# Performance work log

Measured on AMD Instinct MI355X. Metric: run time of the kernel, lower is better.

The kernel has to match this reference:

```python
import jax, jax.numpy as jnp
import numpy as np
import math

D = 256; H = 8; L = 6; DK = D // H

def _ln(x, g, b):
    m = jnp.mean(x, -1, keepdims=True)
    v = jnp.mean((x - m) ** 2, -1, keepdims=True)
    return (x - m) * jax.lax.rsqrt(v + 1e-5) * g + b

def setup_inputs() -> dict:
    key = jax.random.key(0)
    ks = jax.random.split(key, 16)
    B, N, F, E = 8, 768, 128, 4
    s = 0.02
    inp = {}
    inp['node_feats'] = jax.random.normal(ks[0], (B, N, F), jnp.float32)
    inp['adj'] = jax.random.randint(ks[1], (B, N, N), 0, 2, jnp.int32)
    inp['dist'] = jax.random.uniform(ks[2], (B, N, N), jnp.float32)
    inp['edge_type_oh'] = jax.random.uniform(ks[3], (B, N, N, E), jnp.float32)
    inp['node_proj_w'] = jax.random.normal(ks[4], (F, D), jnp.float32) * s
    inp['node_proj_b'] = jnp.zeros((D,), jnp.float32)
    inp['cls'] = jax.random.normal(ks[5], (1, 1, D), jnp.float32) * s
    inp['etw'] = jax.random.normal(ks[6], (E,), jnp.float32) * s
    inp['noedge_bias'] = jnp.float32(-2.0)
    inp['deg_scale'] = jnp.float32(0.2)
    inp['gamma'] = jnp.float32(0.8)
    inp['v2n'] = jnp.float32(0.1)
    inp['n2v'] = jnp.float32(0.1)
    inp['vself'] = jnp.float32(0.05)
    inp['ln1_g'] = jnp.ones((L, D), jnp.float32); inp['ln1_b'] = jnp.zeros((L, D), jnp.float32)
    inp['qw'] = jax.random.normal(ks[7], (L, D, D), jnp.float32) * s; inp['qb'] = jnp.zeros((L, D), jnp.float32)
    inp['kw'] = jax.random.normal(ks[8], (L, D, D), jnp.float32) * s; inp['kb'] = jnp.zeros((L, D), jnp.float32)
    inp['vw'] = jax.random.normal(ks[9], (L, D, D), jnp.float32) * s; inp['vb'] = jnp.zeros((L, D), jnp.float32)
    inp['ow'] = jax.random.normal(ks[10], (L, D, D), jnp.float32) * s; inp['ob'] = jnp.zeros((L, D), jnp.float32)
    inp['ln2_g'] = jnp.ones((L, D), jnp.float32); inp['ln2_b'] = jnp.zeros((L, D), jnp.float32)
    Dm = int(D * 1.0)  # mlp_ratio=1.0
    inp['fc1w'] = jax.random.normal(ks[11], (L, D, Dm), jnp.float32) * s; inp['fc1b'] = jnp.zeros((L, Dm), jnp.float32)
    inp['fc2w'] = jax.random.normal(ks[12], (L, Dm, D), jnp.float32) * s; inp['fc2b'] = jnp.zeros((L, D), jnp.float32)
    return inp

def _build_bias(adj_f, dist, edge_type_oh, etw, noedge_bias, deg_scale, gamma, v2n, n2v, vself):
    # DynamicAttnBiasBuilder: hard_mask=False, use_degree=True, vnode_spd_mode='replace', gamma != 0
    B, N, _ = adj_f.shape
    T = N + 1
    e = jnp.einsum('bije,e->bij', edge_type_oh, etw) - gamma * dist  # (B,N,N)
    e = jnp.where(adj_f > 0, e, e + noedge_bias)
    deg = adj_f.sum(-1)  # (B,N)
    deg_norm = (deg[:, :, None] + deg[:, None, :]) / (deg.max(axis=1, keepdims=True)[:, :, None] + 1e-6)
    e = e + deg_scale * deg_norm
    bias = jnp.zeros((B, T, T), jnp.float32)
    bias = bias.at[:, 1:, 1:].set(e)
    bias = bias.at[:, 0, 1:].set(v2n)   # vnode_spd_mode == 'replace'
    bias = bias.at[:, 1:, 0].set(n2v)
    bias = bias.at[:, 0, 0].set(vself)
    return bias  # (B,T,T), broadcast over heads

def _mhsa(x, bias, qw, qb, kw, kb, vw, vb, ow, ob):
    B, T, _ = x.shape
    q = (x @ qw + qb).reshape(B, T, H, DK).transpose(0, 2, 1, 3)
    k = (x @ kw + kb).reshape(B, T, H, DK).transpose(0, 2, 1, 3)
    v = (x @ vw + vb).reshape(B, T, H, DK).transpose(0, 2, 1, 3)
    scores = jnp.einsum('bhqd,bhkd->bhqk', q, k) / math.sqrt(DK)
    scores = scores + bias[:, None, :, :]
    attn = jax.nn.softmax(scores, axis=-1)
    out = jnp.einsum('bhqk,bhkd->bhqd', attn, v)
    out = out.transpose(0, 2, 1, 3).reshape(B, T, D)
    return out @ ow + ob

def _forward(node_feats, adj, dist, edge_type_oh, node_proj_w, node_proj_b, cls,
             etw, noedge_bias, deg_scale, gamma, v2n, n2v, vself,
             ln1_g, ln1_b, qw, qb, kw, kb, vw, vb, ow, ob,
             ln2_g, ln2_b, fc1w, fc1b, fc2w, fc2b):
    adj_f = adj.astype(jnp.float32)
    bias = _build_bias(adj_f, dist, edge_type_oh, etw, noedge_bias, deg_scale, gamma, v2n, n2v, vself)
    B = node_feats.shape[0]
    x = node_feats @ node_proj_w + node_proj_b  # (B,N,D)
    x = jnp.concatenate([jnp.broadcast_to(cls, (B, 1, D)), x], axis=1)  # prepend virtual node -> (B,T,D)
    for l in range(L):
        h = _mhsa(_ln(x, ln1_g[l], ln1_b[l]), bias, qw[l], qb[l], kw[l], kb[l], vw[l], vb[l], ow[l], ob[l])
        x = x + h
        m = _ln(x, ln2_g[l], ln2_b[l])
        m = jax.nn.gelu(m @ fc1w[l] + fc1b[l], approximate=False) @ fc2w[l] + fc2b[l]
        x = x + m
    return x

def reference(node_feats, adj, dist, edge_type_oh, node_proj_w, node_proj_b, cls,
              etw, noedge_bias, deg_scale, gamma, v2n, n2v, vself,
              ln1_g, ln1_b, qw, qb, kw, kb, vw, vb, ow, ob,
              ln2_g, ln2_b, fc1w, fc1b, fc2w, fc2b):
    return _forward(node_feats, adj, dist, edge_type_oh, node_proj_w, node_proj_b, cls,
                    etw, noedge_bias, deg_scale, gamma, v2n, n2v, vself,
                    ln1_g, ln1_b, qw, qb, kw, kb, vw, vb, ow, ob,
                    ln2_g, ln2_b, fc1w, fc1b, fc2w, fc2b)
```

## Files before the change

kernel.cpp:

```cpp
#include <hip/hip_runtime.h>
#include <math.h>

#define BB 8
#define NN 768
#define TT 769
#define DD 256
#define HH 8
#define DKK 32
#define FF 128
#define LL 6
#define MM 6152
#define SCALE 0.17677669529663687f
#define TP 832
#define GBP 776
#define BSP 792
#define HP 264
#define WSZ 65536

typedef __attribute__((ext_vector_type(8))) short s16x8;
typedef __attribute__((ext_vector_type(8))) unsigned short u16x8;
typedef __attribute__((ext_vector_type(4))) float f32x4;

__device__ inline short f2bf(float x) {
    unsigned u = __float_as_uint(x);
    unsigned r = (u + 0x7FFFu + ((u >> 16) & 1u)) >> 16;
    return (short)r;
}
__device__ inline float bf2f(unsigned short s) {
    return __uint_as_float(((unsigned)s) << 16);
}
__device__ inline float gelu_f(float x) {
    return 0.5f * x * (1.f + erff(x * 0.70710678118654752f));
}

__global__ __launch_bounds__(256) void deg_kernel(const int* __restrict__ adj,
                                                  float* __restrict__ deg) {
    int row  = blockIdx.x * 4 + (threadIdx.x >> 6);
    int lane = threadIdx.x & 63;
    const int* p = adj + (size_t)row * NN;
    int s = 0;
#pragma unroll
    for (int i = 0; i < NN / 64; ++i) s += p[lane + 64 * i];
#pragma unroll
    for (int off = 32; off > 0; off >>= 1) s += __shfl_xor(s, off);
    if (lane == 0) deg[row] = (float)s;
}

__global__ __launch_bounds__(256) void degmax_kernel(const float* __restrict__ deg,
                                                     float* __restrict__ dmax) {
    __shared__ float red[256];
    int b = blockIdx.x, t = threadIdx.x;
    float m = 0.f;
    for (int i = t; i < NN; i += 256) m = fmaxf(m, deg[b * NN + i]);
    red[t] = m;
    __syncthreads();
    for (int s = 128; s > 0; s >>= 1) {
        if (t < s) red[t] = fmaxf(red[t], red[t + s]);
        __syncthreads();
    }
    if (t == 0) dmax[b] = red[0];
}

__global__ __launch_bounds__(256) void bias_kernel(
    const float* __restrict__ dist, const float* __restrict__ eoh,
    const int* __restrict__ adj, const float* __restrict__ deg,
    const float* __restrict__ dmax, const float* __restrict__ etw,
    const float* __restrict__ noedge, const float* __restrict__ degsc,
    const float* __restrict__ gamma, const float* __restrict__ v2n,
    const float* __restrict__ n2v, const float* __restrict__ vself,
    unsigned short* __restrict__ bias)
{
    long long idx = (long long)blockIdx.x * 256 + threadIdx.x;
    const long long total = (long long)BB * TT * GBP;
    if (idx >= total) return;
    int b  = (int)(idx / ((long long)TT * GBP));
    int r  = (int)(idx % ((long long)TT * GBP));
    int qi = r / GBP, kj = r % GBP;
    float out;
    if (kj >= TT)                out = 0.f;
    else if (qi == 0 && kj == 0) out = vself[0];
    else if (qi == 0)            out = v2n[0];
    else if (kj == 0)            out = n2v[0];
    else {
        int i = qi - 1, j = kj - 1;
        size_t e = ((size_t)b * NN + i) * NN + j;
        float4 oh = *(const float4*)(eoh + 4 * e);
        float val = oh.x * etw[0] + oh.y * etw[1] + oh.z * etw[2] + oh.w * etw[3]
                    - gamma[0] * dist[e];
        if (adj[e] == 0) val += noedge[0];
        val += degsc[0] * (deg[b * NN + i] + deg[b * NN + j]) / (dmax[b] + 1e-6f);
        out = val;
    }
    bias[idx] = (unsigned short)f2bf(out);
}

__global__ __launch_bounds__(256) void nodeproj_ln_kernel(
    const float* __restrict__ nf, const float* __restrict__ w,
    const float* __restrict__ bsv, const float* __restrict__ cls,
    const float* __restrict__ g, const float* __restrict__ bvec,
    float* __restrict__ x, short* __restrict__ xn)
{
    __shared__ float sf[FF];
    __shared__ float red[256];
    int row = blockIdx.x, t = threadIdx.x;
    int b = row / TT, tr = row % TT;
    float y;
    if (tr == 0) {
        y = cls[t];
    } else {
        if (t < FF) sf[t] = nf[((size_t)b * NN + tr - 1) * FF + t];
        __syncthreads();
        y = bsv[t];
#pragma unroll 8
        for (int kk = 0; kk < FF; ++kk) y = fmaf(sf[kk], w[kk * DD + t], y);
    }
    x[(size_t)row * DD + t] = y;
    red[t] = y;
    __syncthreads();
    for (int s = 128; s > 0; s >>= 1) { if (t < s) red[t] += red[t + s]; __syncthreads(); }
    float mean = red[0] * (1.f / DD);
    __syncthreads();
    float d = y - mean;
    red[t] = d * d;
    __syncthreads();
    for (int s = 128; s > 0; s >>= 1) { if (t < s) red[t] += red[t + s]; __syncthreads(); }
    float var = red[0] * (1.f / DD);
    xn[(size_t)row * DD + t] = f2bf(d * rsqrtf(var + 1e-5f) * g[t] + bvec[t]);
}

__global__ __launch_bounds__(256) void wtrans_kernel(
    const float* __restrict__ qw, const float* __restrict__ kw,
    const float* __restrict__ vw, const float* __restrict__ ow,
    const float* __restrict__ f1w, const float* __restrict__ f2w,
    short* __restrict__ wt2)
{
    int mi = blockIdx.x >> 4, kg = blockIdx.x & 15;
    int fam = mi / 6, l = mi % 6;
    const float* W;
    if      (fam == 0) W = qw;
    else if (fam == 1) W = kw;
    else if (fam == 2) W = vw;
    else if (fam == 3) W = ow;
    else if (fam == 4) W = f1w;
    else               W = f2w;
    W += (size_t)l * DD * DD;
    int n = threadIdx.x;
    short* out = wt2 + (size_t)mi * WSZ;
#pragma unroll
    for (int kk = 0; kk < 16; ++kk) {
        int k = kg * 16 + kk;
        float val = W[(size_t)k * DD + n];
        size_t idx = (size_t)(((n >> 4) * 8 + (k >> 5)) * 512
                   + (((k >> 3) & 3) * 16 + (n & 15)) * 8 + (k & 7));
        out[idx] = f2bf(val);
    }
}

__global__ __launch_bounds__(256) void gemm_qkv_kernel(
    const short* __restrict__ A, const short* __restrict__ wtl,
    const float* __restrict__ qb, const float* __restrict__ kb,
    const float* __restrict__ vb,
    short* __restrict__ qo, short* __restrict__ ko, short* __restrict__ vtb)
{
    int t = threadIdx.x;
    int w = t >> 6, lane = t & 63, quad = lane >> 4, m16 = lane & 15;
    int m0 = blockIdx.x * 16;
    int fam = blockIdx.y;
    const short* Wf = wtl + (size_t)fam * 6 * WSZ;
    const float* bsv = fam == 0 ? qb : (fam == 1 ? kb : vb);
    int arow = m0 + m16; if (arow >= MM) arow = MM - 1;
    const short* ap = A + (size_t)arow * DD + quad * 8;
    const short* wbase = Wf + (size_t)(w * 4) * 4096 + lane * 8;
    f32x4 acc[4] = {};
#pragma unroll
    for (int kc = 0; kc < 8; ++kc) {
        s16x8 af = *(const s16x8*)(ap + kc * 32);
#pragma unroll
        for (int nt = 0; nt < 4; ++nt) {
            s16x8 bf = *(const s16x8*)(wbase + (size_t)nt * 4096 + kc * 512);
            acc[nt] = __builtin_amdgcn_mfma_f32_16x16x32_bf16(af, bf, acc[nt], 0, 0, 0);
        }
    }
    if (fam < 2) {
        short* outp = fam == 0 ? qo : ko;
#pragma unroll
        for (int nt = 0; nt < 4; ++nt) {
            int col = w * 64 + nt * 16 + m16;
            float bv = bsv[col];
#pragma unroll
            for (int r = 0; r < 4; ++r) {
                int row = m0 + quad * 4 + r;
                if (row < MM) outp[(size_t)row * DD + col] = f2bf(acc[nt][r] + bv);
            }
        }
    } else {
#pragma unroll
        for (int nt = 0; nt < 4; ++nt) {
            int col = w * 64 + nt * 16 + m16;
            float bv = bsv[col];
            int h = col >> 5, dk = col & 31;
#pragma unroll
            for (int r = 0; r < 4; ++r) {
                int row = m0 + quad * 4 + r;
                if (row < MM) {
                    int b = row / TT;
                    int tpos = row - b * TT;
                    vtb[(((size_t)(b * HH + h)) * DKK + dk) * TP + tpos] =
                        f2bf(acc[nt][r] + bv);
                }
            }
        }
    }
}

__global__ __launch_bounds__(256) void attn_kernel(
    const short* __restrict__ q, const short* __restrict__ k,
    const short* __restrict__ vt, const unsigned short* __restrict__ bias,
    short* __restrict__ o)
{
    __shared__ unsigned short bs[16 * BSP];
    __shared__ short Pb[4][16][72];
    int t = threadIdx.x;
    int wid = t >> 6, lane = t & 63;
    int quad = lane >> 4, m16 = lane & 15;
    int bx = blockIdx.x;
    int h4 = bx / 392;
    int rem = bx - h4 * 392;
    int b = rem / 49;
    int qt = rem - b * 49;
    int h = h4 * 4 + wid;
    int q0 = qt * 16;

    for (int i = t; i < 16 * 97; i += 256) {
        int row = i / 97, c8 = (i - row * 97) * 8;
        int qr = q0 + row; if (qr >= TT) qr = TT - 1;
        *(u16x8*)&bs[row * BSP + c8] =
            *(const u16x8*)(bias + ((size_t)(b * TT + qr)) * GBP + c8);
    }

    int qrow = q0 + m16;
    int qc = qrow < TT ? qrow : TT - 1;
    s16x8 qa = *(const s16x8*)(q + ((size_t)(b * TT + qc)) * DD + h * DKK + quad * 8);

    const short* kbase = k + ((size_t)(b * TT)) * DD + h * DKK + quad * 8;
    const short* vbase = vt + (((size_t)(b * HH + h)) * DKK) * TP;

    s16x8 kfA[4], kfB[4], vfA[4], vfB[4];
    f32x4 sacc[4];
    f32x4 o0 = {0.f, 0.f, 0.f, 0.f};
    f32x4 o1 = {0.f, 0.f, 0.f, 0.f};
    float ls[4] = {0.f, 0.f, 0.f, 0.f};

#define LOADK_(DST, CC)                                                         \
    {                                                                           \
        _Pragma("unroll") for (int s = 0; s < 4; ++s) {                         \
            int kr = (CC) * 64 + s * 16 + m16;                                  \
            int kcl = kr < TT ? kr : TT - 1;                                    \
            DST[s] = *(const s16x8*)(kbase + (size_t)kcl * DD);                 \
        }                                                                       \
    }
#define LOADV_(DST, CC)                                                         \
    {                                                                           \
        int jn = (CC) * 64;                                                     \
        DST[0] = *(const s16x8*)(vbase + (size_t)m16 * TP + jn + quad * 8);     \
        DST[1] = *(const s16x8*)(vbase + (size_t)m16 * TP + jn + 32 + quad * 8);\
        DST[2] = *(const s16x8*)(vbase + (size_t)(16 + m16) * TP + jn + quad * 8);\
        DST[3] = *(const s16x8*)(vbase + (size_t)(16 + m16) * TP + jn + 32 + quad * 8);\
    }
#define STEP_(C, KPRE, KUSE, VUSE, VPRE, DOPREK, DOPREV, DOQK)                  \
    {                                                                           \
        if (DOPREK) LOADK_(KPRE, (C) + 2);                                      \
        if (DOPREV) LOADV_(VPRE, (C) + 1);                                      \
        int j0 = (C) * 64;                                                      \
        _Pragma("unroll") for (int s = 0; s < 4; ++s) {                         \
            int key = j0 + s * 16 + m16;                                        \
            int kv = key < TT;                                                  \
            int kidx = kv ? key : 0;                                            \
            _Pragma("unroll") for (int r = 0; r < 4; ++r) {                     \
                float bv = bf2f(bs[(quad * 4 + r) * BSP + kidx]);               \
                float sval = kv ? fmaf(sacc[s][r], SCALE, bv) : -1e30f;         \
                float p = __expf(sval - 8.0f);                                  \
                ls[r] += p;                                                     \
                Pb[wid][quad * 4 + r][s * 16 + m16] = f2bf(p);                  \
            }                                                                   \
        }                                                                       \
        if (DOQK) {                                                             \
            f32x4 z = {0.f, 0.f, 0.f, 0.f};                                     \
            _Pragma("unroll") for (int s = 0; s < 4; ++s)                       \
                sacc[s] = __builtin_amdgcn_mfma_f32_16x16x32_bf16(qa, KUSE[s], z, 0, 0, 0); \
        }                                                                       \
        s16x8 pa0 = *(const s16x8*)&Pb[wid][m16][quad * 8];                     \
        s16x8 pa1 = *(const s16x8*)&Pb[wid][m16][32 + quad * 8];                \
        o0 = __builtin_amdgcn_mfma_f32_16x16x32_bf16(pa0, VUSE[0], o0, 0, 0, 0);\
        o0 = __builtin_amdgcn_mfma_f32_16x16x32_bf16(pa1, VUSE[1], o0, 0, 0, 0);\
        o1 = __builtin_amdgcn_mfma_f32_16x16x32_bf16(pa0, VUSE[2], o1, 0, 0, 0);\
        o1 = __builtin_amdgcn_mfma_f32_16x16x32_bf16(pa1, VUSE[3], o1, 0, 0, 0);\
    }

    LOADK_(kfA, 0);
    LOADK_(kfB, 1);
    LOADV_(vfA, 0);
    {
        f32x4 z = {0.f, 0.f, 0.f, 0.f};
#pragma unroll
        for (int s = 0; s < 4; ++s)
            sacc[s] = __builtin_amdgcn_mfma_f32_16x16x32_bf16(qa, kfA[s], z, 0, 0, 0);
    }
    __syncthreads();

    for (int cc = 0; cc < 5; ++cc) {
        STEP_(2 * cc,     kfA, kfB, vfA, vfB, 1, 1, 1)
        STEP_(2 * cc + 1, kfB, kfA, vfB, vfA, 1, 1, 1)
    }
    STEP_(10, kfA, kfB, vfA, vfB, 1, 1, 1)
    STEP_(11, kfB, kfA, vfB, vfA, 0, 1, 1)
    STEP_(12, kfA, kfB, vfA, vfB, 0, 0, 0)

#undef STEP_
#undef LOADV_
#undef LOADK_

#pragma unroll
    for (int r = 0; r < 4; ++r) {
        float l = ls[r];
#pragma unroll
        for (int off = 1; off < 16; off <<= 1) l += __shfl_xor(l, off);
        int qr = q0 + quad * 4 + r;
        if (qr < TT) {
            float inv = 1.f / l;
            short* op = o + ((size_t)(b * TT + qr)) * DD + h * DKK;
            op[m16]      = f2bf(o0[r] * inv);
            op[16 + m16] = f2bf(o1[r] * inv);
        }
    }
}

__global__ __launch_bounds__(256) void gemm_oln2_kernel(
    const short* __restrict__ A, const short* __restrict__ Ws,
    const float* __restrict__ bsv, const float* __restrict__ g2,
    const float* __restrict__ b2, float* __restrict__ x, short* __restrict__ xn)
{
    __shared__ float redS[64], redQ[64];
    int t = threadIdx.x;
    int w = t >> 6, lane = t & 63, quad = lane >> 4, m16 = lane & 15;
    int m0 = blockIdx.x * 16;
    int arow = m0 + m16; if (arow >= MM) arow = MM - 1;
    const short* ap = A + (size_t)arow * DD + quad * 8;
    const short* wbase = Ws + (size_t)(w * 4) * 4096 + lane * 8;
    f32x4 acc[4] = {};
#pragma unroll
    for (int kc = 0; kc < 8; ++kc) {
        s16x8 af = *(const s16x8*)(ap + kc * 32);
#pragma unroll
        for (int nt = 0; nt < 4; ++nt) {
            s16x8 bf = *(const s16x8*)(wbase + (size_t)nt * 4096 + kc * 512);
            acc[nt] = __builtin_amdgcn_mfma_f32_16x16x32_bf16(af, bf, acc[nt], 0, 0, 0);
        }
    }
    float vv[4][4], sr[4], qr2[4];
#pragma unroll
    for (int r = 0; r < 4; ++r) { sr[r] = 0.f; qr2[r] = 0.f; }
#pragma unroll
    for (int nt = 0; nt < 4; ++nt) {
        int col = w * 64 + nt * 16 + m16;
        float bv = bsv[col];
#pragma unroll
        for (int r = 0; r < 4; ++r) {
            int row = m0 + quad * 4 + r; int rc = row < MM ? row : MM - 1;
            float v = acc[nt][r] + bv + x[(size_t)rc * DD + col];
            vv[nt][r] = v; sr[r] += v; qr2[r] += v * v;
        }
    }
#pragma unroll
    for (int r = 0; r < 4; ++r)
#pragma unroll
        for (int off = 1; off < 16; off <<= 1) {
            sr[r]  += __shfl_xor(sr[r], off);
            qr2[r] += __shfl_xor(qr2[r], off);
        }
    if (m16 == 0) {
#pragma unroll
        for (int r = 0; r < 4; ++r) {
            redS[w * 16 + quad * 4 + r] = sr[r];
            redQ[w * 16 + quad * 4 + r] = qr2[r];
        }
    }
    __syncthreads();
#pragma unroll
    for (int r = 0; r < 4; ++r) {
        int rl = quad * 4 + r;
        int row = m0 + rl;
        float fs = redS[rl] + redS[16 + rl] + redS[32 + rl] + redS[48 + rl];
        float fq = redQ[rl] + redQ[16 + rl] + redQ[32 + rl] + redQ[48 + rl];
        float mean = fs * (1.f / DD);
        float var = fq * (1.f / DD) - mean * mean;
        float inv = rsqrtf(var + 1e-5f);
        if (row < MM) {
#pragma unroll
            for (int nt = 0; nt < 4; ++nt) {
                int col = w * 64 + nt * 16 + m16;
                float v = vv[nt][r];
                x[(size_t)row * DD + col] = v;
                xn[(size_t)row * DD + col] = f2bf((v - mean) * inv * g2[col] + b2[col]);
            }
        }
    }
}

__global__ __launch_bounds__(256) void mlp_kernel(
    short* __restrict__ xn, const short* __restrict__ W1s,
    const short* __restrict__ W2s, const float* __restrict__ f1b,
    const float* __restrict__ f2b, float* __restrict__ x,
    const float* __restrict__ g1, const float* __restrict__ b1, int donext)
{
    __shared__ short hbuf[16 * HP];
    __shared__ float redS[64], redQ[64];
    int t = threadIdx.x;
    int w = t >> 6, lane = t & 63, quad = lane >> 4, m16 = lane & 15;
    int m0 = blockIdx.x * 16;
    int arow = m0 + m16; if (arow >= MM) arow = MM - 1;
    const short* ap = xn + (size_t)arow * DD + quad * 8;
    const short* w1base = W1s + (size_t)(w * 4) * 4096 + lane * 8;
    const short* w2base = W2s + (size_t)(w * 4) * 4096 + lane * 8;

    f32x4 acc[4] = {};
#pragma unroll
    for (int kc = 0; kc < 8; ++kc) {
        s16x8 af = *(const s16x8*)(ap + kc * 32);
#pragma unroll
        for (int nt = 0; nt < 4; ++nt) {
            s16x8 bf = *(const s16x8*)(w1base + (size_t)nt * 4096 + kc * 512);
            acc[nt] = __builtin_amdgcn_mfma_f32_16x16x32_bf16(af, bf, acc[nt], 0, 0, 0);
        }
    }
#pragma unroll
    for (int nt = 0; nt < 4; ++nt) {
        int col = w * 64 + nt * 16 + m16;
        float fb = f1b[col];
#pragma unroll
        for (int r = 0; r < 4; ++r)
            hbuf[(quad * 4 + r) * HP + col] = f2bf(gelu_f(acc[nt][r] + fb));
    }
    __syncthreads();

    f32x4 acc2[4] = {};
#pragma unroll
    for (int kc = 0; kc < 8; ++kc) {
        s16x8 af = *(const s16x8*)&hbuf[m16 * HP + kc * 32 + quad * 8];
#pragma unroll
        for (int nt = 0; nt < 4; ++nt) {
            s16x8 bf = *(const s16x8*)(w2base + (size_t)nt * 4096 + kc * 512);
            acc2[nt] = __builtin_amdgcn_mfma_f32_16x16x32_bf16(af, bf, acc2[nt], 0, 0, 0);
        }
    }
    float vv[4][4], sr[4], qr2[4];
#pragma unroll
    for (int r = 0; r < 4; ++r) { sr[r] = 0.f; qr2[r] = 0.f; }
#pragma unroll
    for (int nt = 0; nt < 4; ++nt) {
        int col = w * 64 + nt * 16 + m16;
        float bv = f2b[col];
#pragma unroll
        for (int r = 0; r < 4; ++r) {
            int row = m0 + quad * 4 + r; int rc = row < MM ? row : MM - 1;
            float v = acc2[nt][r] + bv + x[(size_t)rc * DD + col];
            vv[nt][r] = v; sr[r] += v; qr2[r] += v * v;
        }
    }
#pragma unroll
    for (int r = 0; r < 4; ++r)
#pragma unroll
        for (int off = 1; off < 16; off <<= 1) {
            sr[r]  += __shfl_xor(sr[r], off);
            qr2[r] += __shfl_xor(qr2[r], off);
        }
    if (m16 == 0) {
#pragma unroll
        for (int r = 0; r < 4; ++r) {
            redS[w * 16 + quad * 4 + r] = sr[r];
            redQ[w * 16 + quad * 4 + r] = qr2[r];
        }
    }
    __syncthreads();
#pragma unroll
    for (int r = 0; r < 4; ++r) {
        int rl = quad * 4 + r;
        int row = m0 + rl;
        float fs = redS[rl] + redS[16 + rl] + redS[32 + rl] + redS[48 + rl];
        float fq = redQ[rl] + redQ[16 + rl] + redQ[32 + rl] + redQ[48 + rl];
        float mean = fs * (1.f / DD);
        float var = fq * (1.f / DD) - mean * mean;
        float inv = rsqrtf(var + 1e-5f);
        if (row < MM) {
#pragma unroll
            for (int nt = 0; nt < 4; ++nt) {
                int col = w * 64 + nt * 16 + m16;
                float v = vv[nt][r];
                x[(size_t)row * DD + col] = v;
                if (donext)
                    xn[(size_t)row * DD + col] =
                        f2bf((v - mean) * inv * g1[col] + b1[col]);
            }
        }
    }
}

extern "C" void kernel_launch(void* const* d_in, const int* in_sizes, int n_in,
                              void* d_out, int out_size, void* d_ws, size_t ws_size,
                              hipStream_t stream)
{
    const float* node_feats = (const float*)d_in[0];
    const int*   adj        = (const int*)d_in[1];
    const float* dist       = (const float*)d_in[2];
    const float* eoh        = (const float*)d_in[3];
    const float* npw        = (const float*)d_in[4];
    const float* npb        = (const float*)d_in[5];
    const float* cls        = (const float*)d_in[6];
    const float* etw        = (const float*)d_in[7];
    const float* noedge     = (const float*)d_in[8];
    const float* degsc      = (const float*)d_in[9];
    const float* gamma      = (const float*)d_in[10];
    const float* v2n        = (const float*)d_in[11];
    const float* n2v        = (const float*)d_in[12];
    const float* vself      = (const float*)d_in[13];
    const float* ln1g = (const float*)d_in[14];
    const float* ln1b = (const float*)d_in[15];
    const float* qw   = (const float*)d_in[16];
    const float* qb   = (const float*)d_in[17];
    const float* kw   = (const float*)d_in[18];
    const float* kb   = (const float*)d_in[19];
    const float* vw   = (const float*)d_in[20];
    const float* vb   = (const float*)d_in[21];
    const float* ow   = (const float*)d_in[22];
    const float* ob   = (const float*)d_in[23];
    const float* ln2g = (const float*)d_in[24];
    const float* ln2b = (const float*)d_in[25];
    const float* f1w  = (const float*)d_in[26];
    const float* f1b  = (const float*)d_in[27];
    const float* f2w  = (const float*)d_in[28];
    const float* f2b  = (const float*)d_in[29];

    float* x  = (float*)d_out;
    char* ws = (char*)d_ws;
    size_t off = 0;
    unsigned short* bias = (unsigned short*)(ws + off); off += (size_t)BB * TT * GBP * 2;
    float* deg  = (float*)(ws + off); off += (size_t)BB * NN * 4;
    float* dmax = (float*)(ws + off); off += 64;
    short* xn16 = (short*)(ws + off); off += (size_t)MM * DD * 2;
    short* qb16 = (short*)(ws + off); off += (size_t)MM * DD * 2;
    short* kb16 = (short*)(ws + off); off += (size_t)MM * DD * 2;
    short* vtb  = (short*)(ws + off); off += (size_t)BB * HH * DKK * TP * 2;
    short* ab16 = (short*)(ws + off); off += (size_t)MM * DD * 2;
    short* wt2  = (short*)(ws + off); off += (size_t)36 * WSZ * 2;

    deg_kernel<<<(BB * NN) / 4, 256, 0, stream>>>(adj, deg);
    degmax_kernel<<<BB, 256, 0, stream>>>(deg, dmax);

    long long total = (long long)BB * TT * GBP;
    bias_kernel<<<(int)((total + 255) / 256), 256, 0, stream>>>(
        dist, eoh, adj, deg, dmax, etw, noedge, degsc, gamma, v2n, n2v, vself, bias);

    nodeproj_ln_kernel<<<MM, 256, 0, stream>>>(node_feats, npw, npb, cls,
                                               ln1g, ln1b, x, xn16);

    wtrans_kernel<<<576, 256, 0, stream>>>(qw, kw, vw, ow, f1w, f2w, wt2);

    dim3 gqkv(385, 3);
    for (int l = 0; l < LL; ++l) {
        size_t bo = (size_t)l * DD;
        gemm_qkv_kernel<<<gqkv, 256, 0, stream>>>(xn16, wt2 + (size_t)l * WSZ,
                                                  qb + bo, kb + bo, vb + bo,
                                                  qb16, kb16, vtb);
        attn_kernel<<<784, 256, 0, stream>>>(qb16, kb16, vtb, bias, ab16);
        gemm_oln2_kernel<<<385, 256, 0, stream>>>(ab16, wt2 + (size_t)(3 * 6 + l) * WSZ,
                                                  ob + bo, ln2g + bo, ln2b + bo, x, xn16);
        int donext = (l + 1 < LL) ? 1 : 0;
        size_t bn = (size_t)(l + 1 < LL ? l + 1 : 0) * DD;
        mlp_kernel<<<385, 256, 0, stream>>>(xn16, wt2 + (size_t)(4 * 6 + l) * WSZ,
                                            wt2 + (size_t)(5 * 6 + l) * WSZ,
                                            f1b + bo, f2b + bo, x,
                                            ln1g + bn, ln1b + bn, donext);
    }
}
```

Baseline: 792.4 us.

## Enlarge GEMM row tiles to 64 rows per block for weight reuse

The QKV, output-projection+LN and MLP kernels now process four 16-row MFMA tiles per block, loading each weight fragment once and reusing it across the four row tiles. Grid sizes shrink from 385 to 97 blocks. The goal is to cut redundant weight loads from L2. The cost is more accumulator registers, larger LDS in the MLP kernel, and far fewer blocks than CUs, which reduces parallelism.

```diff
diff --git a/kernel.cpp b/kernel.cpp
--- a/kernel.cpp
+++ b/kernel.cpp
@@ -164,52 +164,66 @@
 {
     int t = threadIdx.x;
     int w = t >> 6, lane = t & 63, quad = lane >> 4, m16 = lane & 15;
-    int m0 = blockIdx.x * 16;
+    int m0 = blockIdx.x * 64;
     int fam = blockIdx.y;
     const short* Wf = wtl + (size_t)fam * 6 * WSZ;
     const float* bsv = fam == 0 ? qb : (fam == 1 ? kb : vb);
-    int arow = m0 + m16; if (arow >= MM) arow = MM - 1;
-    const short* ap = A + (size_t)arow * DD + quad * 8;
+    size_t aro[4];
+#pragma unroll
+    for (int mt = 0; mt < 4; ++mt) {
+        int rr = m0 + mt * 16 + m16; if (rr >= MM) rr = MM - 1;
+        aro[mt] = (size_t)rr * DD;
+    }
+    const short* ap = A + quad * 8;
     const short* wbase = Wf + (size_t)(w * 4) * 4096 + lane * 8;
-    f32x4 acc[4] = {};
+    f32x4 acc[4][4] = {};
 #pragma unroll
     for (int kc = 0; kc < 8; ++kc) {
-        s16x8 af = *(const s16x8*)(ap + kc * 32);
-#pragma unroll
-        for (int nt = 0; nt < 4; ++nt) {
-            s16x8 bf = *(const s16x8*)(wbase + (size_t)nt * 4096 + kc * 512);
-            acc[nt] = __builtin_amdgcn_mfma_f32_16x16x32_bf16(af, bf, acc[nt], 0, 0, 0);
+        s16x8 bfr[4];
+#pragma unroll
+        for (int nt = 0; nt < 4; ++nt)
+            bfr[nt] = *(const s16x8*)(wbase + (size_t)nt * 4096 + kc * 512);
+#pragma unroll
+        for (int mt = 0; mt < 4; ++mt) {
+            s16x8 af = *(const s16x8*)(ap + aro[mt] + kc * 32);
+#pragma unroll
+            for (int nt = 0; nt < 4; ++nt)
+                acc[mt][nt] = __builtin_amdgcn_mfma_f32_16x16x32_bf16(af, bfr[nt], acc[mt][nt], 0, 0, 0);
         }
     }
     if (fam < 2) {
         short* outp = fam == 0 ? qo : ko;
 #pragma unroll
-        for (int nt = 0; nt < 4; ++nt) {
-            int col = w * 64 + nt * 16 + m16;
-            float bv = bsv[col];
-#pragma unroll
-            for (int r = 0; r < 4; ++r) {
-                int row = m0 + quad * 4 + r;
-                if (row < MM) outp[(size_t)row * DD + col] = f2bf(acc[nt][r] + bv);
-            }
-        }
+        for (int mt = 0; mt < 4; ++mt)
+#pragma unroll
+            for (int nt = 0; nt < 4; ++nt) {
+                int col = w * 64 + nt * 16 + m16;
+                float bv = bsv[col];
+#pragma unroll
+                for (int r = 0; r < 4; ++r) {
+                    int row = m0 + mt * 16 + quad * 4 + r;
+                    if (row < MM) outp[(size_t)row * DD + col] = f2bf(acc[mt][nt][r] + bv);
+                }
+            }
     } else {
 #pragma unroll
-        for (int nt = 0; nt < 4; ++nt) {
-            int col = w * 64 + nt * 16 + m16;
-            float bv = bsv[col];
-            int h = col >> 5, dk = col & 31;
-#pragma unroll
-            for (int r = 0; r < 4; ++r) {
-                int row = m0 + quad * 4 + r;
-                if (row < MM) {
-                    int b = row / TT;
-                    int tpos = row - b * TT;
-                    vtb[(((size_t)(b * HH + h)) * DKK + dk) * TP + tpos] =
-                        f2bf(acc[nt][r] + bv);
+        for (int mt = 0; mt < 4; ++mt)
+#pragma unroll
+            for (int nt = 0; nt < 4; ++nt) {
+                int col = w * 64 + nt * 16 + m16;
+                float bv = bsv[col];
+                int h = col >> 5, dk = col & 31;
+#pragma unroll
+                for (int r = 0; r < 4; ++r) {
+                    int row = m0 + mt * 16 + quad * 4 + r;
+                    if (row < MM) {
+                        int b = row / TT;
+                        int tpos = row - b * TT;
+                        vtb[(((size_t)(b * HH + h)) * DKK + dk) * TP + tpos] =
+                            f2bf(acc[mt][nt][r] + bv);
+                    }
                 }
             }
-        }
     }
 }
 
@@ -340,71 +354,93 @@
     const float* __restrict__ bsv, const float* __restrict__ g2,
     const float* __restrict__ b2, float* __restrict__ x, short* __restrict__ xn)
 {
-    __shared__ float redS[64], redQ[64];
+    __shared__ float redS[256], redQ[256];
     int t = threadIdx.x;
     int w = t >> 6, lane = t & 63, quad = lane >> 4, m16 = lane & 15;
-    int m0 = blockIdx.x * 16;
-    int arow = m0 + m16; if (arow >= MM) arow = MM - 1;
-    const short* ap = A + (size_t)arow * DD + quad * 8;
+    int m0 = blockIdx.x * 64;
+    size_t aro[4];
+#pragma unroll
+    for (int mt = 0; mt < 4; ++mt) {
+        int rr = m0 + mt * 16 + m16; if (rr >= MM) rr = MM - 1;
+        aro[mt] = (size_t)rr * DD;
+    }
+    const short* ap = A + quad * 8;
     const short* wbase = Ws + (size_t)(w * 4) * 4096 + lane * 8;
-    f32x4 acc[4] = {};
+    f32x4 acc[4][4] = {};
 #pragma unroll
     for (int kc = 0; kc < 8; ++kc) {
-        s16x8 af = *(const s16x8*)(ap + kc * 32);
+        s16x8 bfr[4];
+#pragma unroll
+        for (int nt = 0; nt < 4; ++nt)
+            bfr[nt] = *(const s16x8*)(wbase + (size_t)nt * 4096 + kc * 512);
+#pragma unroll
+        for (int mt = 0; mt < 4; ++mt) {
+            s16x8 af = *(const s16x8*)(ap + aro[mt] + kc * 32);
+#pragma unroll
+            for (int nt = 0; nt < 4; ++nt)
+                acc[mt][nt] = __builtin_amdgcn_mfma_f32_16x16x32_bf16(af, bfr[nt], acc[mt][nt], 0, 0, 0);
+        }
+    }
+    float sr[4][4], q2[4][4];
+#pragma unroll
+    for (int mt = 0; mt < 4; ++mt)
+#pragma unroll
+        for (int r = 0; r < 4; ++r) { sr[mt][r] = 0.f; q2[mt][r] = 0.f; }
+#pragma unroll
+    for (int mt = 0; mt < 4; ++mt)
 #pragma unroll
         for (int nt = 0; nt < 4; ++nt) {
-            s16x8 bf = *(const s16x8*)(wbase + (size_t)nt * 4096 + kc * 512);
-            acc[nt] = __builtin_amdgcn_mfma_f32_16x16x32_bf16(af, bf, acc[nt], 0, 0, 0);
-        }
-    }
-    float vv[4][4], sr[4], qr2[4];
-#pragma unroll
-    for (int r = 0; r < 4; ++r) { sr[r] = 0.f; qr2[r] = 0.f; }
-#pragma unroll
-    for (int nt = 0; nt < 4; ++nt) {
-        int col = w * 64 + nt * 16 + m16;
-        float bv = bsv[col];
+            int col = w * 64 + nt * 16 + m16;
+            float bv = bsv[col];
+#pragma unroll
+            for (int r = 0; r < 4; ++r) {
+                int row = m0 + mt * 16 + quad * 4 + r; int rc = row < MM ? row : MM - 1;
+                float v = acc[mt][nt][r] + bv + x[(size_t)rc * DD + col];
+                acc[mt][nt][r] = v;
+                sr[mt][r] += v; q2[mt][r] += v * v;
+            }
+        }
+#pragma unroll
+    for (int mt = 0; mt < 4; ++mt)
+#pragma unroll
+        for (int r = 0; r < 4; ++r)
+#pragma unroll
+            for (int off = 1; off < 16; off <<= 1) {
+                sr[mt][r] += __shfl_xor(sr[mt][r], off);
+                q2[mt][r] += __shfl_xor(q2[mt][r], off);
+            }
+    if (m16 == 0) {
+#pragma unroll
+        for (int mt = 0; mt < 4; ++mt)
+#pragma unroll
+            for (int r = 0; r < 4; ++r) {
+                int rl = mt * 16 + quad * 4 + r;
+                redS[w * 64 + rl] = sr[mt][r];
+                redQ[w * 64 + rl] = q2[mt][r];
+            }
+    }
+    __syncthreads();
+#pragma unroll
+    for (int mt = 0; mt < 4; ++mt)
 #pragma unroll
         for (int r = 0; r < 4; ++r) {
-            int row = m0 + quad * 4 + r; int rc = row < MM ? row : MM - 1;
-            float v = acc[nt][r] + bv + x[(size_t)rc * DD + col];
-            vv[nt][r] = v; sr[r] += v; qr2[r] += v * v;
-        }
-    }
-#pragma unroll
-    for (int r = 0; r < 4; ++r)
-#pragma unroll
-        for (int off = 1; off < 16; off <<= 1) {
-            sr[r]  += __shfl_xor(sr[r], off);
-            qr2[r] += __shfl_xor(qr2[r], off);
-        }
-    if (m16 == 0) {
-#pragma unroll
-        for (int r = 0; r < 4; ++r) {
-            redS[w * 16 + quad * 4 + r] = sr[r];
-            redQ[w * 16 + quad * 4 + r] = qr2[r];
-        }
-    }
-    __syncthreads();
-#pragma unroll
-    for (int r = 0; r < 4; ++r) {
-        int rl = quad * 4 + r;
-        int row = m0 + rl;
-        float fs = redS[rl] + redS[16 + rl] + redS[32 + rl] + redS[48 + rl];
-        float fq = redQ[rl] + redQ[16 + rl] + redQ[32 + rl] + redQ[48 + rl];
-        float mean = fs * (1.f / DD);
-        float var = fq * (1.f / DD) - mean * mean;
-        float inv = rsqrtf(var + 1e-5f);
-        if (row < MM) {
-#pragma unroll
-            for (int nt = 0; nt < 4; ++nt) {
-                int col = w * 64 + nt * 16 + m16;
-                float v = vv[nt][r];
-                x[(size_t)row * DD + col] = v;
-                xn[(size_t)row * DD + col] = f2bf((v - mean) * inv * g2[col] + b2[col]);
-            }
-        }
-    }
+            int rl = mt * 16 + quad * 4 + r;
+            int row = m0 + rl;
+            float fs = redS[rl] + redS[64 + rl] + redS[128 + rl] + redS[192 + rl];
+            float fq = redQ[rl] + redQ[64 + rl] + redQ[128 + rl] + redQ[192 + rl];
+            float mean = fs * (1.f / DD);
+            float var = fq * (1.f / DD) - mean * mean;
+            float inv = rsqrtf(var + 1e-5f);
+            if (row < MM) {
+#pragma unroll
+                for (int nt = 0; nt < 4; ++nt) {
+                    int col = w * 64 + nt * 16 + m16;
+                    float v = acc[mt][nt][r];
+                    x[(size_t)row * DD + col] = v;
+                    xn[(size_t)row * DD + col] = f2bf((v - mean) * inv * g2[col] + b2[col]);
+                }
+            }
+        }
 }
 
 __global__ __launch_bounds__(256) void mlp_kernel(
@@ -413,96 +449,127 @@
     const float* __restrict__ f2b, float* __restrict__ x,
     const float* __restrict__ g1, const float* __restrict__ b1, int donext)
 {
-    __shared__ short hbuf[16 * HP];
-    __shared__ float redS[64], redQ[64];
+    __shared__ short hbuf[64 * HP];
+    __shared__ float redS[256], redQ[256];
     int t = threadIdx.x;
     int w = t >> 6, lane = t & 63, quad = lane >> 4, m16 = lane & 15;
-    int m0 = blockIdx.x * 16;
-    int arow = m0 + m16; if (arow >= MM) arow = MM - 1;
-    const short* ap = xn + (size_t)arow * DD + quad * 8;
+    int m0 = blockIdx.x * 64;
+    size_t aro[4];
+#pragma unroll
+    for (int mt = 0; mt < 4; ++mt) {
+        int rr = m0 + mt * 16 + m16; if (rr >= MM) rr = MM - 1;
+        aro[mt] = (size_t)rr * DD;
+    }
+    const short* ap = xn + quad * 8;
     const short* w1base = W1s + (size_t)(w * 4) * 4096 + lane * 8;
     const short* w2base = W2s + (size_t)(w * 4) * 4096 + lane * 8;
 
-    f32x4 acc[4] = {};
-#pragma unroll
-    for (int kc = 0; kc < 8; ++kc) {
-        s16x8 af = *(const s16x8*)(ap + kc * 32);
-#pragma unroll
-        for (int nt = 0; nt < 4; ++nt) {
-            s16x8 bf = *(const s16x8*)(w1base + (size_t)nt * 4096 + kc * 512);
-            acc[nt] = __builtin_amdgcn_mfma_f32_16x16x32_bf16(af, bf, acc[nt], 0, 0, 0);
-        }
-    }
-#pragma unroll
-    for (int nt = 0; nt < 4; ++nt) {
-        int col = w * 64 + nt * 16 + m16;
-        float fb = f1b[col];
-#pragma unroll
-        for (int r = 0; r < 4; ++r)
-            hbuf[(quad * 4 + r) * HP + col] = f2bf(gelu_f(acc[nt][r] + fb));
-    }
-    __syncthreads();
-
-    f32x4 acc2[4] = {};
-#pragma unroll
-    for (int kc = 0; kc < 8; ++kc) {
-        s16x8 af = *(const s16x8*)&hbuf[m16 * HP + kc * 32 + quad * 8];
-#pragma unroll
-        for (int nt = 0; nt < 4; ++nt) {
-            s16x8 bf = *(const s16x8*)(w2base + (size_t)nt * 4096 + kc * 512);
-            acc2[nt] = __builtin_amdgcn_mfma_f32_16x16x32_bf16(af, bf, acc2[nt], 0, 0, 0);
-        }
-    }
-    float vv[4][4], sr[4], qr2[4];
-#pragma unroll
-    for (int r = 0; r < 4; ++r) { sr[r] = 0.f; qr2[r] = 0.f; }
-#pragma unroll
-    for (int nt = 0; nt < 4; ++nt) {
-        int col = w * 64 + nt * 16 + m16;
-        float bv = f2b[col];
-#pragma unroll
-        for (int r = 0; r < 4; ++r) {
-            int row = m0 + quad * 4 + r; int rc = row < MM ? row : MM - 1;
-            float v = acc2[nt][r] + bv + x[(size_t)rc * DD + col];
-            vv[nt][r] = v; sr[r] += v; qr2[r] += v * v;
-        }
-    }
-#pragma unroll
-    for (int r = 0; r < 4; ++r)
-#pragma unroll
-        for (int off = 1; off < 16; off <<= 1) {
-            sr[r]  += __shfl_xor(sr[r], off);
-            qr2[r] += __shfl_xor(qr2[r], off);
-        }
-    if (m16 == 0) {
-#pragma unroll
-        for (int r = 0; r < 4; ++r) {
-            redS[w * 16 + quad * 4 + r] = sr[r];
-            redQ[w * 16 + quad * 4 + r] = qr2[r];
-        }
-    }
-    __syncthreads();
-#pragma unroll
-    for (int r = 0; r < 4; ++r) {
-        int rl = quad * 4 + r;
-        int row = m0 + rl;
-        float fs = redS[rl] + redS[16 + rl] + redS[32 + rl] + redS[48 + rl];
-        float fq = redQ[rl] + redQ[16 + rl] + redQ[32 + rl] + redQ[48 + rl];
-        float mean = fs * (1.f / DD);
-        float var = fq * (1.f / DD) - mean * mean;
-        float inv = rsqrtf(var + 1e-5f);
-        if (row < MM) {
+    {
+        f32x4 acc[4][4] = {};
+#pragma unroll
+        for (int kc = 0; kc < 8; ++kc) {
+            s16x8 bfr[4];
+#pragma unroll
+            for (int nt = 0; nt < 4; ++nt)
+                bfr[nt] = *(const s16x8*)(w1base + (size_t)nt * 4096 + kc * 512);
+#pragma unroll
+            for (int mt = 0; mt < 4; ++mt) {
+                s16x8 af = *(const s16x8*)(ap + aro[mt] + kc * 32);
+#pragma unroll
+                for (int nt = 0; nt < 4; ++nt)
+                    acc[mt][nt] = __builtin_amdgcn_mfma_f32_16x16x32_bf16(af, bfr[nt], acc[mt][nt], 0, 0, 0);
+            }
+        }
+#pragma unroll
+        for (int mt = 0; mt < 4; ++mt)
 #pragma unroll
             for (int nt = 0; nt < 4; ++nt) {
                 int col = w * 64 + nt * 16 + m16;
-                float v = vv[nt][r];
-                x[(size_t)row * DD + col] = v;
-                if (donext)
-                    xn[(size_t)row * DD + col] =
-                        f2bf((v - mean) * inv * g1[col] + b1[col]);
-            }
-        }
-    }
+                float fb = f1b[col];
+#pragma unroll
+                for (int r = 0; r < 4; ++r)
+                    hbuf[(mt * 16 + quad * 4 + r) * HP + col] = f2bf(gelu_f(acc[mt][nt][r] + fb));
+            }
+    }
+    __syncthreads();
+
+    f32x4 acc2[4][4] = {};
+#pragma unroll
+    for (int kc = 0; kc < 8; ++kc) {
+        s16x8 bfr[4];
+#pragma unroll
+        for (int nt = 0; nt < 4; ++nt)
+            bfr[nt] = *(const s16x8*)(w2base + (size_t)nt * 4096 + kc * 512);
+#pragma unroll
+        for (int mt = 0; mt < 4; ++mt) {
+            s16x8 af = *(const s16x8*)&hbuf[(mt * 16 + m16) * HP + kc * 32 + quad * 8];
+#pragma unroll
+            for (int nt = 0; nt < 4; ++nt)
+                acc2[mt][nt] = __builtin_amdgcn_mfma_f32_16x16x32_bf16(af, bfr[nt], acc2[mt][nt], 0, 0, 0);
+        }
+    }
+    float sr[4][4], q2[4][4];
+#pragma unroll
+    for (int mt = 0; mt < 4; ++mt)
+#pragma unroll
+        for (int r = 0; r < 4; ++r) { sr[mt][r] = 0.f; q2[mt][r] = 0.f; }
+#pragma unroll
+    for (int mt = 0; mt < 4; ++mt)
+#pragma unroll
+        for (int nt = 0; nt < 4; ++nt) {
+            int col = w * 64 + nt * 16 + m16;
+            float bv = f2b[col];
+#pragma unroll
+            for (int r = 0; r < 4; ++r) {
+                int row = m0 + mt * 16 + quad * 4 + r; int rc = row < MM ? row : MM - 1;
+                float v = acc2[mt][nt][r] + bv + x[(size_t)rc * DD + col];
+                acc2[mt][nt][r] = v;
+                sr[mt][r] += v; q2[mt][r] += v * v;
+            }
+        }
+#pragma unroll
+    for (int mt = 0; mt < 4; ++mt)
+#pragma unroll
+        for (int r = 0; r < 4; ++r)
+#pragma unroll
+            for (int off = 1; off < 16; off <<= 1) {
+                sr[mt][r] += __shfl_xor(sr[mt][r], off);
+                q2[mt][r] += __shfl_xor(q2[mt][r], off);
+            }
+    if (m16 == 0) {
+#pragma unroll
+        for (int mt = 0; mt < 4; ++mt)
+#pragma unroll
+            for (int r = 0; r < 4; ++r) {
+                int rl = mt * 16 + quad * 4 + r;
+                redS[w * 64 + rl] = sr[mt][r];
+                redQ[w * 64 + rl] = q2[mt][r];
+            }
+    }
+    __syncthreads();
+#pragma unroll
+    for (int mt = 0; mt < 4; ++mt)
+#pragma unroll
+        for (int r = 0; r < 4; ++r) {
+            int rl = mt * 16 + quad * 4 + r;
+            int row = m0 + rl;
+            float fs = redS[rl] + redS[64 + rl] + redS[128 + rl] + redS[192 + rl];
+            float fq = redQ[rl] + redQ[64 + rl] + redQ[128 + rl] + redQ[192 + rl];
+            float mean = fs * (1.f / DD);
+            float var = fq * (1.f / DD) - mean * mean;
+            float inv = rsqrtf(var + 1e-5f);
+            if (row < MM) {
+#pragma unroll
+                for (int nt = 0; nt < 4; ++nt) {
+                    int col = w * 64 + nt * 16 + m16;
+                    float v = acc2[mt][nt][r];
+                    x[(size_t)row * DD + col] = v;
+                    if (donext)
+                        xn[(size_t)row * DD + col] =
+                            f2bf((v - mean) * inv * g1[col] + b1[col]);
+                }
+            }
+        }
 }
 
 extern "C" void kernel_launch(void* const* d_in, const int* in_sizes, int n_in,
@@ -565,20 +632,20 @@
 
     wtrans_kernel<<<576, 256, 0, stream>>>(qw, kw, vw, ow, f1w, f2w, wt2);
 
-    dim3 gqkv(385, 3);
+    dim3 gqkv(97, 3);
     for (int l = 0; l < LL; ++l) {
         size_t bo = (size_t)l * DD;
         gemm_qkv_kernel<<<gqkv, 256, 0, stream>>>(xn16, wt2 + (size_t)l * WSZ,
                                                   qb + bo, kb + bo, vb + bo,
                                                   qb16, kb16, vtb);
         attn_kernel<<<784, 256, 0, stream>>>(qb16, kb16, vtb, bias, ab16);
-        gemm_oln2_kernel<<<385, 256, 0, stream>>>(ab16, wt2 + (size_t)(3 * 6 + l) * WSZ,
-                                                  ob + bo, ln2g + bo, ln2b + bo, x, xn16);
+        gemm_oln2_kernel<<<97, 256, 0, stream>>>(ab16, wt2 + (size_t)(3 * 6 + l) * WSZ,
+                                                 ob + bo, ln2g + bo, ln2b + bo, x, xn16);
         int donext = (l + 1 < LL) ? 1 : 0;
         size_t bn = (size_t)(l + 1 < LL ? l + 1 : 0) * DD;
-        mlp_kernel<<<385, 256, 0, stream>>>(xn16, wt2 + (size_t)(4 * 6 + l) * WSZ,
-                                            wt2 + (size_t)(5 * 6 + l) * WSZ,
-                                            f1b + bo, f2b + bo, x,
-                                            ln1g + bn, ln1b + bn, donext);
-    }
-}
+        mlp_kernel<<<97, 256, 0, stream>>>(xn16, wt2 + (size_t)(4 * 6 + l) * WSZ,
+                                           wt2 + (size_t)(5 * 6 + l) * WSZ,
+                                           f1b + bo, f2b + bo, x,
+                                           ln1g + bn, ln1b + bn, donext);
+    }
+}
```

After: 942.7 us. +19.0%, slower.

## Store Q/K head-major and stream attention bias from global into registers

Applied to the files above, without the earlier changes.

The QKV GEMM now writes Q and K in a per-(batch, head) layout of contiguous 32-wide rows, so each attention wave reads K rows at a stride of 64 bytes instead of 512. The attention kernel no longer stages the 16-row bias tile in shared memory behind a block barrier. Each lane instead prefetches its bias values from global memory into double-buffered registers one chunk ahead. This removes the shared-memory tile and the __syncthreads. The cost is scattered 2-byte global loads for the bias, which all four head-waves in a block now fetch separately, plus higher register pressure.

```diff
diff --git a/kernel.cpp b/kernel.cpp
--- a/kernel.cpp
+++ b/kernel.cpp
@@ -12,8 +12,9 @@
 #define MM 6152
 #define SCALE 0.17677669529663687f
 #define TP 832
+#define KQP 784
+#define KHS (KQP * DKK)
 #define GBP 776
-#define BSP 792
 #define HP 264
 #define WSZ 65536
 
@@ -160,7 +161,7 @@
     const short* __restrict__ A, const short* __restrict__ wtl,
     const float* __restrict__ qb, const float* __restrict__ kb,
     const float* __restrict__ vb,
-    short* __restrict__ qo, short* __restrict__ ko, short* __restrict__ vtb)
+    short* __restrict__ qh, short* __restrict__ kh, short* __restrict__ vtb)
 {
     int t = threadIdx.x;
     int w = t >> 6, lane = t & 63, quad = lane >> 4, m16 = lane & 15;
@@ -182,15 +183,21 @@
         }
     }
     if (fam < 2) {
-        short* outp = fam == 0 ? qo : ko;
-#pragma unroll
-        for (int nt = 0; nt < 4; ++nt) {
-            int col = w * 64 + nt * 16 + m16;
-            float bv = bsv[col];
-#pragma unroll
-            for (int r = 0; r < 4; ++r) {
-                int row = m0 + quad * 4 + r;
-                if (row < MM) outp[(size_t)row * DD + col] = f2bf(acc[nt][r] + bv);
+        short* outp = fam == 0 ? qh : kh;
+#pragma unroll
+        for (int r = 0; r < 4; ++r) {
+            int row = m0 + quad * 4 + r;
+            if (row < MM) {
+                int b = row / TT;
+                int tpos = row - b * TT;
+                size_t rb = ((size_t)b * HH * KQP + tpos) * DKK;
+#pragma unroll
+                for (int nt = 0; nt < 4; ++nt) {
+                    int col = w * 64 + nt * 16 + m16;
+                    float bv = bsv[col];
+                    int h = col >> 5, dk = col & 31;
+                    outp[rb + (size_t)h * KHS + dk] = f2bf(acc[nt][r] + bv);
+                }
             }
         }
     } else {
@@ -218,7 +225,6 @@
     const short* __restrict__ vt, const unsigned short* __restrict__ bias,
     short* __restrict__ o)
 {
-    __shared__ unsigned short bs[16 * BSP];
     __shared__ short Pb[4][16][72];
     int t = threadIdx.x;
     int wid = t >> 6, lane = t & 63;
@@ -231,21 +237,23 @@
     int h = h4 * 4 + wid;
     int q0 = qt * 16;
 
-    for (int i = t; i < 16 * 97; i += 256) {
-        int row = i / 97, c8 = (i - row * 97) * 8;
-        int qr = q0 + row; if (qr >= TT) qr = TT - 1;
-        *(u16x8*)&bs[row * BSP + c8] =
-            *(const u16x8*)(bias + ((size_t)(b * TT + qr)) * GBP + c8);
+    size_t rb4[4];
+#pragma unroll
+    for (int r = 0; r < 4; ++r) {
+        int qr = q0 + quad * 4 + r; if (qr >= TT) qr = TT - 1;
+        rb4[r] = (size_t)(b * TT + qr) * GBP;
     }
 
     int qrow = q0 + m16;
     int qc = qrow < TT ? qrow : TT - 1;
-    s16x8 qa = *(const s16x8*)(q + ((size_t)(b * TT + qc)) * DD + h * DKK + quad * 8);
-
-    const short* kbase = k + ((size_t)(b * TT)) * DD + h * DKK + quad * 8;
+    const short* qbase = q + (size_t)(b * HH + h) * KHS;
+    s16x8 qa = *(const s16x8*)(qbase + (size_t)qc * DKK + quad * 8);
+
+    const short* kbase = k + (size_t)(b * HH + h) * KHS;
     const short* vbase = vt + (((size_t)(b * HH + h)) * DKK) * TP;
 
     s16x8 kfA[4], kfB[4], vfA[4], vfB[4];
+    unsigned short bbA[16], bbB[16];
     f32x4 sacc[4];
     f32x4 o0 = {0.f, 0.f, 0.f, 0.f};
     f32x4 o1 = {0.f, 0.f, 0.f, 0.f};
@@ -256,7 +264,7 @@
         _Pragma("unroll") for (int s = 0; s < 4; ++s) {                         \
             int kr = (CC) * 64 + s * 16 + m16;                                  \
             int kcl = kr < TT ? kr : TT - 1;                                    \
-            DST[s] = *(const s16x8*)(kbase + (size_t)kcl * DD);                 \
+            DST[s] = *(const s16x8*)(kbase + (size_t)kcl * DKK + quad * 8);     \
         }                                                                       \
     }
 #define LOADV_(DST, CC)                                                         \
@@ -267,17 +275,26 @@
         DST[2] = *(const s16x8*)(vbase + (size_t)(16 + m16) * TP + jn + quad * 8);\
         DST[3] = *(const s16x8*)(vbase + (size_t)(16 + m16) * TP + jn + 32 + quad * 8);\
     }
-#define STEP_(C, KPRE, KUSE, VUSE, VPRE, DOPREK, DOPREV, DOQK)                  \
+#define LOADB_(DST, CC)                                                         \
+    {                                                                           \
+        _Pragma("unroll") for (int s = 0; s < 4; ++s) {                         \
+            int ko = (CC) * 64 + s * 16 + m16;                                  \
+            ko = ko < TT ? ko : 0;                                              \
+            _Pragma("unroll") for (int r = 0; r < 4; ++r)                       \
+                DST[s * 4 + r] = bias[rb4[r] + ko];                             \
+        }                                                                       \
+    }
+#define STEP_(C, KPRE, KUSE, VUSE, VPRE, BUSE, BPRE, DOPREK, DOPREV, DOPREB, DOQK) \
     {                                                                           \
         if (DOPREK) LOADK_(KPRE, (C) + 2);                                      \
         if (DOPREV) LOADV_(VPRE, (C) + 1);                                      \
+        if (DOPREB) LOADB_(BPRE, (C) + 1);                                      \
         int j0 = (C) * 64;                                                      \
         _Pragma("unroll") for (int s = 0; s < 4; ++s) {                         \
             int key = j0 + s * 16 + m16;                                        \
             int kv = key < TT;                                                  \
-            int kidx = kv ? key : 0;                                            \
             _Pragma("unroll") for (int r = 0; r < 4; ++r) {                     \
-                float bv = bf2f(bs[(quad * 4 + r) * BSP + kidx]);               \
+                float bv = bf2f(BUSE[s * 4 + r]);                               \
                 float sval = kv ? fmaf(sacc[s][r], SCALE, bv) : -1e30f;         \
                 float p = __expf(sval - 8.0f);                                  \
                 ls[r] += p;                                                     \
@@ -300,23 +317,24 @@
     LOADK_(kfA, 0);
     LOADK_(kfB, 1);
     LOADV_(vfA, 0);
+    LOADB_(bbA, 0);
     {
         f32x4 z = {0.f, 0.f, 0.f, 0.f};
 #pragma unroll
         for (int s = 0; s < 4; ++s)
             sacc[s] = __builtin_amdgcn_mfma_f32_16x16x32_bf16(qa, kfA[s], z, 0, 0, 0);
     }
-    __syncthreads();
 
     for (int cc = 0; cc < 5; ++cc) {
-        STEP_(2 * cc,     kfA, kfB, vfA, vfB, 1, 1, 1)
-        STEP_(2 * cc + 1, kfB, kfA, vfB, vfA, 1, 1, 1)
-    }
-    STEP_(10, kfA, kfB, vfA, vfB, 1, 1, 1)
-    STEP_(11, kfB, kfA, vfB, vfA, 0, 1, 1)
-    STEP_(12, kfA, kfB, vfA, vfB, 0, 0, 0)
+        STEP_(2 * cc,     kfA, kfB, vfA, vfB, bbA, bbB, 1, 1, 1, 1)
+        STEP_(2 * cc + 1, kfB, kfA, vfB, vfA, bbB, bbA, 1, 1, 1, 1)
+    }
+    STEP_(10, kfA, kfB, vfA, vfB, bbA, bbB, 1, 1, 1, 1)
+    STEP_(11, kfB, kfA, vfB, vfA, bbB, bbA, 0, 1, 1, 1)
+    STEP_(12, kfA, kfB, vfA, vfB, bbA, bbB, 0, 0, 0, 0)
 
 #undef STEP_
+#undef LOADB_
 #undef LOADV_
 #undef LOADK_
 
@@ -547,8 +565,8 @@
     float* deg  = (float*)(ws + off); off += (size_t)BB * NN * 4;
     float* dmax = (float*)(ws + off); off += 64;
     short* xn16 = (short*)(ws + off); off += (size_t)MM * DD * 2;
-    short* qb16 = (short*)(ws + off); off += (size_t)MM * DD * 2;
-    short* kb16 = (short*)(ws + off); off += (size_t)MM * DD * 2;
+    short* qhb  = (short*)(ws + off); off += (size_t)BB * HH * KQP * DKK * 2;
+    short* khb  = (short*)(ws + off); off += (size_t)BB * HH * KQP * DKK * 2;
     short* vtb  = (short*)(ws + off); off += (size_t)BB * HH * DKK * TP * 2;
     short* ab16 = (short*)(ws + off); off += (size_t)MM * DD * 2;
     short* wt2  = (short*)(ws + off); off += (size_t)36 * WSZ * 2;
@@ -570,8 +588,8 @@
         size_t bo = (size_t)l * DD;
         gemm_qkv_kernel<<<gqkv, 256, 0, stream>>>(xn16, wt2 + (size_t)l * WSZ,
                                                   qb + bo, kb + bo, vb + bo,
-                                                  qb16, kb16, vtb);
-        attn_kernel<<<784, 256, 0, stream>>>(qb16, kb16, vtb, bias, ab16);
+                                                  qhb, khb, vtb);
+        attn_kernel<<<784, 256, 0, stream>>>(qhb, khb, vtb, bias, ab16);
         gemm_oln2_kernel<<<385, 256, 0, stream>>>(ab16, wt2 + (size_t)(3 * 6 + l) * WSZ,
                                                   ob + bo, ln2g + bo, ln2b + bo, x, xn16);
         int donext = (l + 1 < LL) ? 1 : 0;
```

After: 751.2 us. -5.2%, faster.
